# Performance work log

Measured on AMD Instinct MI355X. Metric: run time of the kernel, lower is better.

## Reference

```python
import jax, jax.numpy as jnp
import numpy as np

NUM_HEADS = 4

def setup_inputs() -> dict:
    key = jax.random.key(0)
    ks = jax.random.split(key, 5)
    B, N, C = 2, 4096, 256
    s = 0.02
    return {
        "x": jax.random.normal(ks[0], (B, N, C), dtype=jnp.float32),
        "qkv_w": jax.random.normal(ks[1], (3 * C, C), dtype=jnp.float32) * s,
        "qkv_b": jax.random.normal(ks[2], (3 * C,), dtype=jnp.float32) * s,
        "out_w": jax.random.normal(ks[3], (C, C), dtype=jnp.float32) * s,
        "out_b": jax.random.normal(ks[4], (C,), dtype=jnp.float32) * s,
    }

def reference(x, qkv_w, qkv_b, out_w, out_b):
    # x: [B, N, C]; manual multi-head self-attention (eval mode, dropout off)
    B, N, C = x.shape
    H = NUM_HEADS
    D = C // H
    qkv = x @ qkv_w.T + qkv_b                      # [B, N, 3C]
    qkv = qkv.reshape(B, N, 3, H, D)
    qkv = jnp.transpose(qkv, (2, 0, 3, 1, 4))      # [3, B, H, N, D]
    q, k, v = qkv[0], qkv[1], qkv[2]
    scale = D ** -0.5
    attn = jnp.einsum('bhnd,bhmd->bhnm', q, k) * scale  # [B, H, N, N]
    attn = jax.nn.softmax(attn, axis=-1)
    out = jnp.einsum('bhnm,bhmd->bhnd', attn, v)   # [B, H, N, D]
    out = jnp.transpose(out, (0, 2, 1, 3)).reshape(B, N, C)
    return out @ out_w.T + out_b
```

## Files before the change

### kernel.cpp

```cpp
#include <hip/hip_runtime.h>

typedef __bf16 bf16x8 __attribute__((ext_vector_type(8)));
typedef float f32x4 __attribute__((ext_vector_type(4)));

#define MFMA_BF16(a, b, c) __builtin_amdgcn_mfma_f32_16x16x32_bf16((a), (b), (c), 0, 0, 0)

#define C1 0.18033688f

static __device__ __forceinline__ unsigned short f2bf(float f) {
    unsigned int u = __float_as_uint(f);
    unsigned int r = (u + 0x7fffu + ((u >> 16) & 1u)) >> 16;
    return (unsigned short)r;
}
static __device__ __forceinline__ float bf2f(unsigned short us) {
    return __uint_as_float(((unsigned int)us) << 16);
}
static __device__ __forceinline__ float exp2_hw(float x) {
    float r;
    asm("v_exp_f32 %0, %1" : "=v"(r) : "v"(x));
    return r;
}
static __device__ __forceinline__ unsigned pack_rh(float a, float b) {
    return __byte_perm(__float_as_uint(a) + 0x8000u, __float_as_uint(b) + 0x8000u, 0x7632);
}
static __device__ __forceinline__ void gload16(const void* g, void* l) {
    __builtin_amdgcn_global_load_lds(
        (const __attribute__((address_space(1))) unsigned int*)g,
        (__attribute__((address_space(3))) unsigned int*)l, 16, 0, 0);
}

static __device__ __forceinline__ void conv_seg8(const void* src, unsigned short* dst, int n,
                                                 int lb, bool f32) {
    const int base = lb * 2048 + (int)threadIdx.x * 8;
    if (base < n) {
        if (f32) {
            const float4 u0 = *(const float4*)((const float*)src + base);
            const float4 u1 = *(const float4*)((const float*)src + base + 4);
            uint4 p;
            p.x = pack_rh(u0.x, u0.y);
            p.y = pack_rh(u0.z, u0.w);
            p.z = pack_rh(u1.x, u1.y);
            p.w = pack_rh(u1.z, u1.w);
            *(uint4*)(dst + base) = p;
        } else {
            *(uint4*)(dst + base) = *(const uint4*)((const unsigned short*)src + base);
        }
    }
}

__global__ __launch_bounds__(256) void convert_kernel(
    const void* __restrict__ x, const void* __restrict__ qw, const void* __restrict__ qb,
    const void* __restrict__ ow, const void* __restrict__ ob,
    unsigned short* __restrict__ xb, unsigned short* __restrict__ qwb,
    unsigned short* __restrict__ qbb, unsigned short* __restrict__ owb,
    unsigned short* __restrict__ obb, int* __restrict__ flag) {
    __shared__ int tot;
    if (threadIdx.x == 0) tot = 0;
    __syncthreads();
    {
        unsigned short v = ((const unsigned short*)x)[threadIdx.x];
        int e = (v >> 7) & 0xFF;
        if (e >= 195) atomicAdd(&tot, 1);
    }
    __syncthreads();
    const bool f32 = (tot >= 8);
    if (blockIdx.x == 0 && threadIdx.x == 0) flag[0] = f32 ? 1 : 0;

    const int bid = blockIdx.x;
    if (bid < 1024)       conv_seg8(x,  xb,  2097152, bid,        f32);
    else if (bid < 1120)  conv_seg8(qw, qwb, 196608,  bid - 1024, f32);
    else if (bid < 1121)  conv_seg8(qb, qbb, 768,     bid - 1120, f32);
    else if (bid < 1153)  conv_seg8(ow, owb, 65536,   bid - 1121, f32);
    else                  conv_seg8(ob, obb, 256,     bid - 1153, f32);
}

template <bool QKV>
__global__ __launch_bounds__(256) void gemm_kernel(
    const unsigned short* __restrict__ A, const unsigned short* __restrict__ W,
    const unsigned short* __restrict__ bias, unsigned short* __restrict__ Cb,
    float* __restrict__ Cf, const int* __restrict__ flag,
    unsigned short* __restrict__ Vt, int Nout) {
    constexpr int K = 256;
    __shared__ __align__(16) char sm[16384];

    const int tid = threadIdx.x;
    const int lane = tid & 63;
    const int wv = tid >> 6;
    const int m16 = lane & 15;
    const int quad = lane >> 4;
    const int bm = blockIdx.x * 64;
    const int bn = blockIdx.y * 64;

    int bgo[2], blo[2];
#pragma unroll
    for (int i = 0; i < 2; i++) {
        const int c = wv * 128 + i * 64 + lane;
        const int r = c >> 3, g = (c & 7) ^ (r & 7);
        bgo[i] = r * (K * 2) + g * 16;
        blo[i] = c * 16;
    }
    int bro[4][2];
#pragma unroll
    for (int t = 0; t < 4; t++)
#pragma unroll
        for (int ks = 0; ks < 2; ks++) {
            const int row = t * 16 + m16;
            bro[t][ks] = row * 64 + ((4 * ks + quad) ^ (m16 & 7)) * 8;
        }

    const char* bg = (const char*)(W + (size_t)bn * K);
    const unsigned short* ap = A + (size_t)(bm + wv * 16 + m16) * K + quad * 8;

#pragma unroll
    for (int i = 0; i < 2; i++) gload16(bg + bgo[i], sm + blo[i]);
    bf16x8 a0 = *(const bf16x8*)(ap);
    bf16x8 a1 = *(const bf16x8*)(ap + 32);

    f32x4 acc[4] = {};
#pragma unroll
    for (int kb = 0; kb < 4; kb++) {
        __syncthreads();
        const int cur = kb & 1;
        bf16x8 a0n, a1n;
        if (kb < 3) {
            bg += 128;
            char* Bdst = sm + (cur ^ 1) * 8192;
#pragma unroll
            for (int i = 0; i < 2; i++) gload16(bg + bgo[i], Bdst + blo[i]);
            a0n = *(const bf16x8*)(ap + (kb + 1) * 64);
            a1n = *(const bf16x8*)(ap + (kb + 1) * 64 + 32);
        }
        const unsigned short* Blds = (const unsigned short*)(sm + cur * 8192);
#pragma unroll
        for (int ks = 0; ks < 2; ks++) {
            const bf16x8 a = ks ? a1 : a0;
#pragma unroll
            for (int t = 0; t < 4; t++) {
                const bf16x8 b = *(const bf16x8*)(Blds + bro[t][ks]);
                acc[t] = MFMA_BF16(a, b, acc[t]);
            }
        }
        if (kb < 3) {
            a0 = a0n;
            a1 = a1n;
        }
    }

    if (QKV && bn >= 512) {
        __syncthreads();
        unsigned short* tr = (unsigned short*)sm;
        const int lr = wv * 16 + quad * 4;
#pragma unroll
        for (int t = 0; t < 4; t++) {
            const float bv = bf2f(bias[bn + t * 16 + m16]);
            uint2 w;
            w.x = pack_rh(acc[t][0] + bv, acc[t][1] + bv);
            w.y = pack_rh(acc[t][2] + bv, acc[t][3] + bv);
            *(uint2*)&tr[(t * 16 + m16) * 72 + lr] = w;
        }
        __syncthreads();
        const int d = tid >> 2;
        const int ch = (tid & 3) * 16;
        const uint4 o4a = *(const uint4*)&tr[d * 72 + ch];
        const uint4 o4b = *(const uint4*)&tr[d * 72 + ch + 8];
        const int hh = (bn - 512) >> 6;
        const int bb = bm >> 12, n0 = bm & 4095;
        const int nn = n0 + ch;
        const int kt = nn >> 7, koff = nn & 127;
        unsigned short* vdst =
            &Vt[(size_t)(((bb * 4 + hh) * 32 + kt) * 64 + d) * 128 + koff];
        *(uint4*)(vdst) = o4a;
        *(uint4*)(vdst + 8) = o4b;
        return;
    }

    const bool outf = (!QKV) && (flag != nullptr) && (*flag != 0);
    const int row0 = bm + wv * 16 + quad * 4;
#pragma unroll
    for (int t = 0; t < 4; t++) {
        const int col = bn + t * 16 + m16;
        const float bv = bf2f(bias[col]);
        float v[4];
#pragma unroll
        for (int r = 0; r < 4; r++) v[r] = acc[t][r] + bv;
        if (QKV) {
            const float sc = (col < 256) ? C1 : 1.0f;
#pragma unroll
            for (int r = 0; r < 4; r++)
                Cb[(size_t)(row0 + r) * 768 + col] = f2bf(v[r] * sc);
        } else {
            if (outf) {
#pragma unroll
                for (int r = 0; r < 4; r++) Cf[(size_t)(row0 + r) * Nout + col] = v[r];
            } else {
#pragma unroll
                for (int r = 0; r < 4; r++) Cb[(size_t)(row0 + r) * Nout + col] = f2bf(v[r]);
            }
        }
    }
}

__global__ __launch_bounds__(256) void attn_kernel(
    const unsigned short* __restrict__ qkv, const unsigned short* __restrict__ Vt,
    unsigned short* __restrict__ attn, int iters) {
    const int N = 4096, C3 = 768;
    __shared__ __align__(16) char sm[65536];

    const int tid = threadIdx.x;
    const int lane = tid & 63;
    const int wv = tid >> 6;
    const int m16 = lane & 15;
    const int quad = lane >> 4;

    const int bh = blockIdx.x & 7;
    const int qt = blockIdx.x >> 3;
    const int b = bh >> 2, h = bh & 3;

    bf16x8 qf[4][2];
#pragma unroll
    for (int j = 0; j < 4; j++)
#pragma unroll
        for (int ks = 0; ks < 2; ks++)
            qf[j][ks] = *(const bf16x8*)(qkv + ((size_t)b * N + qt * 64 + j * 16 + m16) * C3 +
                                         h * 64 + ks * 32 + quad * 8);

    uint4 ones_u;
    ones_u.x = ones_u.y = ones_u.z = ones_u.w = 0x3F803F80u;
    const bf16x8 ones = *(const bf16x8*)&ones_u;

    int kgo[4], vgo[4], klo[4], vlo[4];
#pragma unroll
    for (int i = 0; i < 4; i++) {
        const int c = i * 64 + lane;
        const int r = c >> 3, g = (c & 7) ^ (r & 7);
        kgo[i] = (wv * 32 + r) * 1536 + g * 16;
        klo[i] = c * 16;
        const int d = c >> 2, js = c & 3, jg = js ^ ((d >> 2) & 3);
        vgo[i] = d * 256 + wv * 64 + jg * 16;
        vlo[i] = c * 16;
    }
    int kro[2][2];
#pragma unroll
    for (int mb = 0; mb < 2; mb++)
#pragma unroll
        for (int ks = 0; ks < 2; ks++) {
            const int row = mb * 16 + m16;
            kro[mb][ks] = row * 64 + ((4 * ks + quad) ^ (m16 & 7)) * 8;
        }
    int vroA[4];
#pragma unroll
    for (int t = 0; t < 4; t++) {
        const int d = t * 16 + m16;
        const int c0 = (quad >> 1) ^ ((d >> 2) & 3);
        vroA[t] = d * 32 + c0 * 8 + (quad & 1) * 4;
    }

    char* Kreg0 = sm + wv * 8192;
    char* Vreg0 = sm + 32768 + wv * 8192;

    const char* kgp = (const char*)(qkv + (size_t)b * N * C3 + 256 + h * 64);
    const char* vgp = (const char*)(Vt + (size_t)bh * 262144);

#pragma unroll
    for (int i = 0; i < 4; i++) gload16(kgp + kgo[i], Kreg0 + klo[i]);
#pragma unroll
    for (int i = 0; i < 4; i++) gload16(vgp + vgo[i], Vreg0 + vlo[i]);
    const char* kgn = kgp + 128 * 1536;
    const char* vgn = vgp + 16384;

    f32x4 o[4][4] = {};
    f32x4 o1[4] = {};

    for (int kt = 0; kt < iters; ++kt) {
        const int cur = kt & 1;
        if (kt + 1 < iters) {
            char* Kdst = Kreg0 + (cur ^ 1) * 4096;
            char* Vdst = Vreg0 + (cur ^ 1) * 4096;
#pragma unroll
            for (int i = 0; i < 4; i++) gload16(kgn + kgo[i], Kdst + klo[i]);
#pragma unroll
            for (int i = 0; i < 4; i++) gload16(vgn + vgo[i], Vdst + vlo[i]);
            kgn += 128 * 1536;
            vgn += 16384;
            asm volatile("s_waitcnt vmcnt(12)" ::: "memory");
        } else {
            asm volatile("s_waitcnt vmcnt(4)" ::: "memory");
        }
        const unsigned short* Kb = (const unsigned short*)(Kreg0 + cur * 4096);
        const unsigned short* Vb = (const unsigned short*)(Vreg0 + cur * 4096);

        f32x4 s[2][4] = {};
        __builtin_amdgcn_s_setprio(1);
#pragma unroll
        for (int mb = 0; mb < 2; mb++)
#pragma unroll
            for (int ks = 0; ks < 2; ks++) {
                const bf16x8 ka = *(const bf16x8*)(Kb + kro[mb][ks]);
#pragma unroll
                for (int j = 0; j < 4; j++) s[mb][j] = MFMA_BF16(ka, qf[j][ks], s[mb][j]);
            }
        __builtin_amdgcn_s_setprio(0);

        bf16x8 pa[4];
#pragma unroll
        for (int j = 0; j < 4; j++) {
            const float e0 = exp2_hw(s[0][j][0]);
            const float e1 = exp2_hw(s[0][j][1]);
            const float e2 = exp2_hw(s[0][j][2]);
            const float e3 = exp2_hw(s[0][j][3]);
            const float e4 = exp2_hw(s[1][j][0]);
            const float e5 = exp2_hw(s[1][j][1]);
            const float e6 = exp2_hw(s[1][j][2]);
            const float e7 = exp2_hw(s[1][j][3]);
            uint4 pw;
            pw.x = pack_rh(e0, e1);
            pw.y = pack_rh(e2, e3);
            pw.z = pack_rh(e4, e5);
            pw.w = pack_rh(e6, e7);
            pa[j] = *(const bf16x8*)&pw;
        }

        if (kt + 1 < iters) {
            asm volatile("s_waitcnt vmcnt(8)" ::: "memory");
        } else {
            asm volatile("s_waitcnt vmcnt(0)" ::: "memory");
        }

        __builtin_amdgcn_s_setprio(1);
#pragma unroll
        for (int j = 0; j < 4; j++) o1[j] = MFMA_BF16(pa[j], ones, o1[j]);
#pragma unroll
        for (int t = 0; t < 4; t++) {
            const uint2 va = *(const uint2*)(Vb + vroA[t]);
            const uint2 vc = *(const uint2*)(Vb + (vroA[t] ^ 16));
            uint4 vv;
            vv.x = va.x;
            vv.y = va.y;
            vv.z = vc.x;
            vv.w = vc.y;
            const bf16x8 vb = *(const bf16x8*)&vv;
#pragma unroll
            for (int j = 0; j < 4; j++) o[j][t] = MFMA_BF16(pa[j], vb, o[j][t]);
        }
        __builtin_amdgcn_s_setprio(0);
    }

    __syncthreads();
    float* Ored = (float*)sm;
    float* lsum = (float*)(sm + 16384);
    if (m16 == 0) {
#pragma unroll
        for (int j = 0; j < 4; j++)
#pragma unroll
            for (int r = 0; r < 4; r++)
                lsum[wv * 64 + j * 16 + quad * 4 + r] = o1[j][r];
    }
    const int row = tid >> 4;
    const int col = (tid & 15) * 4;
#pragma unroll
    for (int j = 0; j < 4; j++) {
#pragma unroll
        for (int t = 0; t < 4; t++)
#pragma unroll
            for (int r = 0; r < 4; r++)
                Ored[(wv * 16 + quad * 4 + r) * 64 + t * 16 + m16] = o[j][t][r];
        __syncthreads();
        f32x4 sum = *(f32x4*)&Ored[row * 64 + col];
        sum += *(f32x4*)&Ored[1024 + row * 64 + col];
        sum += *(f32x4*)&Ored[2048 + row * 64 + col];
        sum += *(f32x4*)&Ored[3072 + row * 64 + col];
        const float lq = lsum[j * 16 + row] + lsum[64 + j * 16 + row] +
                         lsum[128 + j * 16 + row] + lsum[192 + j * 16 + row];
        const int n = qt * 64 + j * 16 + row;
        const float inv = 1.0f / lq;
        uint2 w;
        w.x = pack_rh(sum[0] * inv, sum[1] * inv);
        w.y = pack_rh(sum[2] * inv, sum[3] * inv);
        *(uint2*)&attn[((size_t)b * N + n) * 256 + h * 64 + col] = w;
        __syncthreads();
    }
}

extern "C" void kernel_launch(void* const* d_in, const int* in_sizes, int n_in,
                              void* d_out, int out_size, void* d_ws, size_t ws_size,
                              hipStream_t stream) {
    const int B = 2, N = 4096, H = 4;
    const int M = B * N;

    char* wsb = (char*)d_ws;
    int* flag = (int*)wsb;
    unsigned short* xb      = (unsigned short*)(wsb + 64);
    unsigned short* qwb     = xb + 2097152;
    unsigned short* qbb     = qwb + 196608;
    unsigned short* owb     = qbb + 768;
    unsigned short* obb     = owb + 65536;
    unsigned short* qkv_ws  = obb + 256;
    unsigned short* Vt_ws   = qkv_ws + 6291456;
    unsigned short* attn_ws = Vt_ws + 2097152;

    convert_kernel<<<1154, 256, 0, stream>>>(d_in[0], d_in[1], d_in[2], d_in[3], d_in[4],
                                             xb, qwb, qbb, owb, obb, flag);

    gemm_kernel<true><<<dim3(M / 64, 768 / 64), 256, 0, stream>>>(
        xb, qwb, qbb, qkv_ws, nullptr, nullptr, Vt_ws, 768);

    attn_kernel<<<512, 256, 0, stream>>>(qkv_ws, Vt_ws, attn_ws, 32);

    gemm_kernel<false><<<dim3(M / 64, 256 / 64), 256, 0, stream>>>(
        attn_ws, owb, obb, (unsigned short*)d_out, (float*)d_out, flag, nullptr, 256);
}
```

Measured before the change: 137.7 us.

## Software-pipeline attention loop: overlap next QK^T with current exp and PV

Restructures the attention main loop into a two-stage software pipeline. The next tile's QK^T MFMAs are issued before the exp and PV of the current tile, and the K and V loads are issued separately so K can be refilled earlier. Two tiles are prefetched up front and the loop is manually unrolled by two, with a hardcoded trip count of 15 that ignores the `iters` argument. It also adds a minimum of 2 blocks per CU to the launch bounds. The cost is higher register pressure from the two score buffers, plus a fixed-size assumption.

```diff
diff --git a/kernel.cpp b/kernel.cpp
--- a/kernel.cpp
+++ b/kernel.cpp
@@ -200,7 +200,81 @@
     }
 }
 
-__global__ __launch_bounds__(256) void attn_kernel(
+#define ZERO_S(S)                                                     \
+    do {                                                              \
+        _Pragma("unroll") for (int mb = 0; mb < 2; mb++)              \
+            _Pragma("unroll") for (int j = 0; j < 4; j++)             \
+                S[mb][j] = (f32x4){0.f, 0.f, 0.f, 0.f};               \
+    } while (0)
+
+#define QKT(S, KBASE)                                                          \
+    do {                                                                       \
+        const unsigned short* Kb_ = (const unsigned short*)(KBASE);            \
+        __builtin_amdgcn_s_setprio(1);                                         \
+        _Pragma("unroll") for (int mb = 0; mb < 2; mb++)                       \
+            _Pragma("unroll") for (int ks = 0; ks < 2; ks++) {                 \
+                const bf16x8 ka_ = *(const bf16x8*)(Kb_ + kro[mb][ks]);        \
+                _Pragma("unroll") for (int j = 0; j < 4; j++)                  \
+                    S[mb][j] = MFMA_BF16(ka_, qf[j][ks], S[mb][j]);            \
+            }                                                                  \
+        __builtin_amdgcn_s_setprio(0);                                         \
+    } while (0)
+
+#define EXPP(S, PA)                                                            \
+    do {                                                                       \
+        _Pragma("unroll") for (int j = 0; j < 4; j++) {                        \
+            const float e0 = exp2_hw(S[0][j][0]);                              \
+            const float e1 = exp2_hw(S[0][j][1]);                              \
+            const float e2 = exp2_hw(S[0][j][2]);                              \
+            const float e3 = exp2_hw(S[0][j][3]);                              \
+            const float e4 = exp2_hw(S[1][j][0]);                              \
+            const float e5 = exp2_hw(S[1][j][1]);                              \
+            const float e6 = exp2_hw(S[1][j][2]);                              \
+            const float e7 = exp2_hw(S[1][j][3]);                              \
+            uint4 pw_;                                                         \
+            pw_.x = pack_rh(e0, e1);                                           \
+            pw_.y = pack_rh(e2, e3);                                           \
+            pw_.z = pack_rh(e4, e5);                                           \
+            pw_.w = pack_rh(e6, e7);                                           \
+            PA[j] = *(const bf16x8*)&pw_;                                      \
+        }                                                                      \
+    } while (0)
+
+#define PVACC(PA, VBASE)                                                       \
+    do {                                                                       \
+        const unsigned short* Vb_ = (const unsigned short*)(VBASE);            \
+        __builtin_amdgcn_s_setprio(1);                                         \
+        _Pragma("unroll") for (int j = 0; j < 4; j++)                          \
+            o1[j] = MFMA_BF16(PA[j], ones, o1[j]);                             \
+        _Pragma("unroll") for (int t = 0; t < 4; t++) {                        \
+            const uint2 va_ = *(const uint2*)(Vb_ + vroA[t]);                  \
+            const uint2 vc_ = *(const uint2*)(Vb_ + (vroA[t] ^ 16));           \
+            uint4 vv_;                                                         \
+            vv_.x = va_.x;                                                     \
+            vv_.y = va_.y;                                                     \
+            vv_.z = vc_.x;                                                     \
+            vv_.w = vc_.y;                                                     \
+            const bf16x8 vb_ = *(const bf16x8*)&vv_;                           \
+            _Pragma("unroll") for (int j = 0; j < 4; j++)                      \
+                o[j][t] = MFMA_BF16(PA[j], vb_, o[j][t]);                      \
+        }                                                                      \
+        __builtin_amdgcn_s_setprio(0);                                         \
+    } while (0)
+
+#define GLK(DST)                                                               \
+    {                                                                          \
+        _Pragma("unroll") for (int i = 0; i < 4; i++)                          \
+            gload16(kgn + kgo[i], (DST) + klo[i]);                             \
+        kgn += 196608;                                                         \
+    }
+#define GLV(DST)                                                               \
+    {                                                                          \
+        _Pragma("unroll") for (int i = 0; i < 4; i++)                          \
+            gload16(vgn + vgo[i], (DST) + vlo[i]);                             \
+        vgn += 16384;                                                          \
+    }
+
+__global__ __launch_bounds__(256, 2) void attn_kernel(
     const unsigned short* __restrict__ qkv, const unsigned short* __restrict__ Vt,
     unsigned short* __restrict__ attn, int iters) {
     const int N = 4096, C3 = 768;
@@ -265,85 +339,49 @@
     for (int i = 0; i < 4; i++) gload16(kgp + kgo[i], Kreg0 + klo[i]);
 #pragma unroll
     for (int i = 0; i < 4; i++) gload16(vgp + vgo[i], Vreg0 + vlo[i]);
-    const char* kgn = kgp + 128 * 1536;
-    const char* vgn = vgp + 16384;
+#pragma unroll
+    for (int i = 0; i < 4; i++) gload16(kgp + 196608 + kgo[i], Kreg0 + 4096 + klo[i]);
+#pragma unroll
+    for (int i = 0; i < 4; i++) gload16(vgp + 16384 + vgo[i], Vreg0 + 4096 + vlo[i]);
+    const char* kgn = kgp + 2 * 196608;
+    const char* vgn = vgp + 2 * 16384;
 
     f32x4 o[4][4] = {};
     f32x4 o1[4] = {};
-
-    for (int kt = 0; kt < iters; ++kt) {
-        const int cur = kt & 1;
-        if (kt + 1 < iters) {
-            char* Kdst = Kreg0 + (cur ^ 1) * 4096;
-            char* Vdst = Vreg0 + (cur ^ 1) * 4096;
-#pragma unroll
-            for (int i = 0; i < 4; i++) gload16(kgn + kgo[i], Kdst + klo[i]);
-#pragma unroll
-            for (int i = 0; i < 4; i++) gload16(vgn + vgo[i], Vdst + vlo[i]);
-            kgn += 128 * 1536;
-            vgn += 16384;
-            asm volatile("s_waitcnt vmcnt(12)" ::: "memory");
-        } else {
-            asm volatile("s_waitcnt vmcnt(4)" ::: "memory");
-        }
-        const unsigned short* Kb = (const unsigned short*)(Kreg0 + cur * 4096);
-        const unsigned short* Vb = (const unsigned short*)(Vreg0 + cur * 4096);
-
-        f32x4 s[2][4] = {};
-        __builtin_amdgcn_s_setprio(1);
-#pragma unroll
-        for (int mb = 0; mb < 2; mb++)
-#pragma unroll
-            for (int ks = 0; ks < 2; ks++) {
-                const bf16x8 ka = *(const bf16x8*)(Kb + kro[mb][ks]);
-#pragma unroll
-                for (int j = 0; j < 4; j++) s[mb][j] = MFMA_BF16(ka, qf[j][ks], s[mb][j]);
-            }
-        __builtin_amdgcn_s_setprio(0);
-
-        bf16x8 pa[4];
-#pragma unroll
-        for (int j = 0; j < 4; j++) {
-            const float e0 = exp2_hw(s[0][j][0]);
-            const float e1 = exp2_hw(s[0][j][1]);
-            const float e2 = exp2_hw(s[0][j][2]);
-            const float e3 = exp2_hw(s[0][j][3]);
-            const float e4 = exp2_hw(s[1][j][0]);
-            const float e5 = exp2_hw(s[1][j][1]);
-            const float e6 = exp2_hw(s[1][j][2]);
-            const float e7 = exp2_hw(s[1][j][3]);
-            uint4 pw;
-            pw.x = pack_rh(e0, e1);
-            pw.y = pack_rh(e2, e3);
-            pw.z = pack_rh(e4, e5);
-            pw.w = pack_rh(e6, e7);
-            pa[j] = *(const bf16x8*)&pw;
-        }
-
-        if (kt + 1 < iters) {
-            asm volatile("s_waitcnt vmcnt(8)" ::: "memory");
-        } else {
-            asm volatile("s_waitcnt vmcnt(0)" ::: "memory");
-        }
-
-        __builtin_amdgcn_s_setprio(1);
-#pragma unroll
-        for (int j = 0; j < 4; j++) o1[j] = MFMA_BF16(pa[j], ones, o1[j]);
-#pragma unroll
-        for (int t = 0; t < 4; t++) {
-            const uint2 va = *(const uint2*)(Vb + vroA[t]);
-            const uint2 vc = *(const uint2*)(Vb + (vroA[t] ^ 16));
-            uint4 vv;
-            vv.x = va.x;
-            vv.y = va.y;
-            vv.z = vc.x;
-            vv.w = vc.y;
-            const bf16x8 vb = *(const bf16x8*)&vv;
-#pragma unroll
-            for (int j = 0; j < 4; j++) o[j][t] = MFMA_BF16(pa[j], vb, o[j][t]);
-        }
-        __builtin_amdgcn_s_setprio(0);
-    }
+    f32x4 sA[2][4], sB[2][4];
+    bf16x8 pa[4];
+
+    asm volatile("s_waitcnt vmcnt(12)" ::: "memory");
+    ZERO_S(sA);
+    QKT(sA, Kreg0);
+
+    for (int t2 = 0; t2 < 15; ++t2) {
+        asm volatile("s_waitcnt vmcnt(4)" ::: "memory");
+        GLK(Kreg0);
+        ZERO_S(sB);
+        QKT(sB, Kreg0 + 4096);
+        EXPP(sA, pa);
+        PVACC(pa, Vreg0);
+        asm volatile("s_waitcnt lgkmcnt(0)" ::: "memory");
+        GLV(Vreg0);
+
+        asm volatile("s_waitcnt vmcnt(4)" ::: "memory");
+        GLK(Kreg0 + 4096);
+        ZERO_S(sA);
+        QKT(sA, Kreg0);
+        EXPP(sB, pa);
+        PVACC(pa, Vreg0 + 4096);
+        asm volatile("s_waitcnt lgkmcnt(0)" ::: "memory");
+        GLV(Vreg0 + 4096);
+    }
+    asm volatile("s_waitcnt vmcnt(4)" ::: "memory");
+    ZERO_S(sB);
+    QKT(sB, Kreg0 + 4096);
+    EXPP(sA, pa);
+    PVACC(pa, Vreg0);
+    asm volatile("s_waitcnt vmcnt(0)" ::: "memory");
+    EXPP(sB, pa);
+    PVACC(pa, Vreg0 + 4096);
 
     __syncthreads();
     float* Ored = (float*)sm;
```

Result: faster. 133.7 us (-2.9%).
